# Kernel optimization log

Hardware: AMD Instinct MI355X
Metric: run time of the kernel (lower is better)

The kernel has to match this reference:

```python
import jax, jax.numpy as jnp
import numpy as np

B, N, D = 8, 2048, 256
TOP_K_INST = 512
TOP_K_REL = 32
EPS = 1e-5  # F.layer_norm default eps


def setup_inputs() -> dict:
    key = jax.random.key(0)
    kq, kk = jax.random.split(key)
    q = jax.random.normal(kq, (B, N, D), dtype=jnp.float32)
    k = jax.random.normal(kk, (B, N, D), dtype=jnp.float32)
    return {"q": q, "k": k}


def _forward(q, k):
    # raw attention scores [B,N,N] (returned un-normalized, like scores1 in torch)
    scores1 = jnp.einsum('bid,bjd->bij', q, k)
    probs = jax.nn.softmax(scores1, axis=-1)
    # top-k instances by softmax self-score on the diagonal, sorted ascending
    diag = jnp.diagonal(probs, axis1=-2, axis2=-1)                      # [B,N]
    inst_idx = jnp.sort(jax.lax.top_k(diag, TOP_K_INST)[1], axis=-1)    # [B,K]
    # gather selected rows then selected columns -> [B,K,K]
    sel = jnp.take_along_axis(probs, inst_idx[:, :, None], axis=1)      # [B,K,N]
    rel = jnp.take_along_axis(sel, inst_idx[:, None, :], axis=2)        # [B,K,K]
    # mask diagonal with large value (torch uses 1e9) before relationship topk
    rel = jnp.where(jnp.eye(TOP_K_INST, dtype=bool)[None, :, :], 1e9, rel)
    # top-R relationship columns per row; torch.where recovers them in
    # ascending column order, so sort to match
    rel_idx = jnp.sort(jax.lax.top_k(rel, TOP_K_REL)[1], axis=-1)       # [B,K,R]
    b, K, R = rel_idx.shape
    rows = jnp.broadcast_to(jnp.arange(K)[None, :, None], (b, K, R)).reshape(b, K * R)
    cols = rel_idx.reshape(b, K * R)
    subj = jnp.take_along_axis(inst_idx, rows, axis=-1)                 # [B,K*R]
    obj = jnp.take_along_axis(inst_idx, cols, axis=-1)                  # [B,K*R]
    batch_ids = jnp.broadcast_to(jnp.arange(b)[:, None], (b, K * R))
    soi = jnp.stack([batch_ids, subj, obj], axis=-1)                    # [B,K*R,3]
    # relationship embeds: q[subject] + q[object], then layernorm (no affine)
    subj_e = jnp.take_along_axis(q, subj[:, :, None], axis=1)           # [B,K*R,D]
    obj_e = jnp.take_along_axis(q, obj[:, :, None], axis=1)
    rel_e = subj_e + obj_e
    mu = jnp.mean(rel_e, axis=-1, keepdims=True)
    var = jnp.var(rel_e, axis=-1, keepdims=True)  # biased, matches F.layer_norm
    rel_e = (rel_e - mu) * jax.lax.rsqrt(var + EPS)
    return scores1, soi, rel_e


def reference(q, k):
    return _forward(q, k)
```

## Files before the change

kernel.cpp:

```cpp
#include <hip/hip_runtime.h>
#include <math.h>

#define BATCH 8
#define N 2048
#define D 256
#define K_INST 512
#define K_REL 32
#define PAIRS_PER_B (K_INST * K_REL)

__device__ __forceinline__ unsigned short f2h_u(float f) {
  _Float16 h = (_Float16)f;
  return __builtin_bit_cast(unsigned short, h);
}
__device__ __forceinline__ float h2f_u(unsigned short u) {
  return (float)__builtin_bit_cast(_Float16, u);
}

__global__ __launch_bounds__(256)
void split_f16(const float* __restrict__ q, const float* __restrict__ k,
               unsigned short* __restrict__ qhs, unsigned short* __restrict__ qh,
               unsigned short* __restrict__ ql, unsigned short* __restrict__ kh,
               unsigned short* __restrict__ kl) {
  const int E4 = BATCH * N * D / 4;
  for (int i = blockIdx.x * blockDim.x + threadIdx.x; i < 2 * E4;
       i += gridDim.x * blockDim.x) {
    const bool isK = i >= E4;
    const int j = isK ? (i - E4) : i;
    const float4 v = ((const float4*)(isK ? k : q))[j];
    ushort4 h, l;
    h.x = f2h_u(v.x); h.y = f2h_u(v.y); h.z = f2h_u(v.z); h.w = f2h_u(v.w);
    l.x = f2h_u(2048.0f * (v.x - h2f_u(h.x)));
    l.y = f2h_u(2048.0f * (v.y - h2f_u(h.y)));
    l.z = f2h_u(2048.0f * (v.z - h2f_u(h.z)));
    l.w = f2h_u(2048.0f * (v.w - h2f_u(h.w)));
    if (isK) {
      ((ushort4*)kh)[j] = h;
      ((ushort4*)kl)[j] = l;
    } else {
      ushort4 hs;
      hs.x = f2h_u(2048.0f * h2f_u(h.x));
      hs.y = f2h_u(2048.0f * h2f_u(h.y));
      hs.z = f2h_u(2048.0f * h2f_u(h.z));
      hs.w = f2h_u(2048.0f * h2f_u(h.w));
      ((ushort4*)qhs)[j] = hs;
      ((ushort4*)qh)[j] = h;
      ((ushort4*)ql)[j] = l;
    }
  }
}

#define TM 128
#define TN 128
#define TK 32

typedef _Float16 f16x8 __attribute__((ext_vector_type(8)));
typedef float f32x4 __attribute__((ext_vector_type(4)));

__device__ __forceinline__ void load_lds16(const void* g, void* l) {
  __builtin_amdgcn_global_load_lds(
      (const __attribute__((address_space(1))) void*)g,
      (__attribute__((address_space(3))) void*)l, 16, 0, 0);
}

__global__ __launch_bounds__(256, 3)
void gemm_qkT_mfma(const unsigned short* __restrict__ qhs,
                   const unsigned short* __restrict__ qh,
                   const unsigned short* __restrict__ ql,
                   const unsigned short* __restrict__ kh,
                   const unsigned short* __restrict__ kl,
                   float* __restrict__ out) {
  const int bz = blockIdx.z;
  const int row0 = blockIdx.y * TM;
  const int col0 = blockIdx.x * TN;
  const size_t tb = (size_t)bz * N * D;

  __shared__ unsigned short Ahs[TM * TK], Ah[TM * TK], Al[TM * TK],
                            Bh[TM * TK], Bl[TM * TK];

  const int tid = threadIdx.x;
  const int lane = tid & 63;
  const int w = tid >> 6;
  const int wr = w >> 1, wc = w & 1;
  const int fr = lane & 15;
  const int g = lane >> 4;
  const int slot8 = ((g ^ (lane & 3)) << 3);

  int r_st[2], k_st[2];
#pragma unroll
  for (int i = 0; i < 2; i++) {
    const int b = ((w * 2 + i) << 10) + lane * 16;
    const int r = b >> 6;
    const int s = (b >> 4) & 3;
    r_st[i] = r;
    k_st[i] = (s ^ (r & 3)) * 8;
  }

  f32x4 acc[4][4];
#pragma unroll
  for (int m = 0; m < 4; m++)
#pragma unroll
    for (int n = 0; n < 4; n++) acc[m][n] = (f32x4){0.f, 0.f, 0.f, 0.f};

  for (int kt = 0; kt < D; kt += TK) {
    __syncthreads();
#pragma unroll
    for (int i = 0; i < 2; i++) {
      const size_t aoff = tb + (size_t)(row0 + r_st[i]) * D + kt + k_st[i];
      const size_t boff = tb + (size_t)(col0 + r_st[i]) * D + kt + k_st[i];
      const int ldsoff = (w * 2 + i) * 512;
      load_lds16(qhs + aoff, &Ahs[ldsoff]);
      load_lds16(qh  + aoff, &Ah[ldsoff]);
      load_lds16(ql  + aoff, &Al[ldsoff]);
      load_lds16(kh  + boff, &Bh[ldsoff]);
      load_lds16(kl  + boff, &Bl[ldsoff]);
    }
    __syncthreads();

    f16x8 ahs[4], ah[4], al[4];
#pragma unroll
    for (int m = 0; m < 4; m++) {
      const int idx = (wr * 64 + m * 16 + fr) * TK + slot8;
      ahs[m] = *(const f16x8*)&Ahs[idx];
      ah[m] = *(const f16x8*)&Ah[idx];
      al[m] = *(const f16x8*)&Al[idx];
    }
#pragma unroll
    for (int n = 0; n < 4; n++) {
      const int idx = (wc * 64 + n * 16 + fr) * TK + slot8;
      const f16x8 bhf = *(const f16x8*)&Bh[idx];
      const f16x8 blf = *(const f16x8*)&Bl[idx];
#pragma unroll
      for (int m = 0; m < 4; m++) {
        acc[m][n] = __builtin_amdgcn_mfma_f32_16x16x32_f16(ahs[m], bhf, acc[m][n], 0, 0, 0);
        acc[m][n] = __builtin_amdgcn_mfma_f32_16x16x32_f16(ah[m], blf, acc[m][n], 0, 0, 0);
        acc[m][n] = __builtin_amdgcn_mfma_f32_16x16x32_f16(al[m], bhf, acc[m][n], 0, 0, 0);
      }
    }
  }

  float* O = out + (size_t)bz * N * N;
  const float inv2048 = 1.0f / 2048.0f;
#pragma unroll
  for (int m = 0; m < 4; m++) {
#pragma unroll
    for (int r4 = 0; r4 < 4; r4++) {
      float* orow =
          &O[(size_t)(row0 + wr * 64 + m * 16 + g * 4 + r4) * N + col0 + wc * 64 + fr];
#pragma unroll
      for (int n = 0; n < 4; n++) orow[n * 16] = acc[m][n][r4] * inv2048;
    }
  }
}

__global__ __launch_bounds__(256)
void row_stats(const float* __restrict__ scores, float* __restrict__ m_out,
               float* __restrict__ s_out, float* __restrict__ diag_out) {
  const int row = blockIdx.x;
  const float* srow = scores + (size_t)row * N;
  const float4* r4 = (const float4*)srow;
  const int t = threadIdx.x;
  const int lane = t & 63, wid = t >> 6;
  float4 v0 = r4[t];
  float4 v1 = r4[t + 256];
  float mx = fmaxf(fmaxf(fmaxf(v0.x, v0.y), fmaxf(v0.z, v0.w)),
                   fmaxf(fmaxf(v1.x, v1.y), fmaxf(v1.z, v1.w)));
  __shared__ float redm[4], reds[4], bc[1];
#pragma unroll
  for (int o = 32; o > 0; o >>= 1) mx = fmaxf(mx, __shfl_down(mx, o));
  if (lane == 0) redm[wid] = mx;
  __syncthreads();
  if (t == 0) bc[0] = fmaxf(fmaxf(redm[0], redm[1]), fmaxf(redm[2], redm[3]));
  __syncthreads();
  const float m = bc[0];
  float s = expf(v0.x - m) + expf(v0.y - m) + expf(v0.z - m) + expf(v0.w - m)
          + expf(v1.x - m) + expf(v1.y - m) + expf(v1.z - m) + expf(v1.w - m);
#pragma unroll
  for (int o = 32; o > 0; o >>= 1) s += __shfl_down(s, o);
  if (lane == 0) reds[wid] = s;
  __syncthreads();
  if (t == 0) {
    float S = reds[0] + reds[1] + reds[2] + reds[3];
    int i = row & (N - 1);
    float sii = srow[i];
    m_out[row] = m;
    s_out[row] = S;
    diag_out[row] = expf(sii - m) / S;
  }
}

__global__ __launch_bounds__(1024)
void topk_inst(const float* __restrict__ diag, int* __restrict__ inst) {
  const int b = blockIdx.x;
  __shared__ float v[2048];
  __shared__ int id[2048];
  __shared__ int sel[K_INST];
  const int tid = threadIdx.x;
  for (int e = tid; e < 2048; e += 1024) { v[e] = diag[b * N + e]; id[e] = e; }
  __syncthreads();
  for (int k = 2; k <= 2048; k <<= 1) {
    for (int j = k >> 1; j > 0; j >>= 1) {
      const int p = tid;
      int i = 2 * p - (p & (j - 1));
      int ixj = i | j;
      float va = v[i], vb = v[ixj];
      int ia = id[i], ib = id[ixj];
      bool a_first = (va > vb) || (va == vb && ia < ib);
      bool up = ((i & k) == 0);
      if (up != a_first) { v[i] = vb; v[ixj] = va; id[i] = ib; id[ixj] = ia; }
      __syncthreads();
    }
  }
  if (tid < K_INST) sel[tid] = id[tid];
  __syncthreads();
  for (int k = 2; k <= K_INST; k <<= 1) {
    for (int j = k >> 1; j > 0; j >>= 1) {
      if (tid < 256) {
        int p = tid;
        int i = 2 * p - (p & (j - 1));
        int ixj = i | j;
        int a = sel[i], c = sel[ixj];
        bool a_first = a < c;
        bool up = ((i & k) == 0);
        if (up != a_first) { sel[i] = c; sel[ixj] = a; }
      }
      __syncthreads();
    }
  }
  if (tid < K_INST) inst[b * K_INST + tid] = sel[tid];
}

__global__ __launch_bounds__(256)
void rel_topk(const float* __restrict__ scores, const int* __restrict__ inst,
              float* __restrict__ soi_out, int* __restrict__ pairs) {
  const int blk = blockIdx.x;
  const int b = blk >> 9;
  const int r = blk & 511;
  __shared__ unsigned long long kv[K_INST];
  __shared__ int selc[K_REL];
  __shared__ int sortedc[K_REL];
  const int tid = threadIdx.x;
  const int subj = inst[b * K_INST + r];
  const float* srow = scores + ((size_t)b * N + subj) * N;
  for (int e = tid; e < K_INST; e += 256) {
    unsigned int fb;
    if (e == r) {
      fb = 0xFFFFFFFFu;
    } else {
      const int col = inst[b * K_INST + e];
      unsigned int u = __float_as_uint(srow[col]);
      fb = (u >> 31) ? ~u : (u | 0x80000000u);
    }
    kv[e] = ((unsigned long long)fb << 32) | (unsigned int)(K_INST - 1 - e);
  }
  __syncthreads();
  for (int k = 2; k <= K_INST; k <<= 1) {
    for (int j = k >> 1; j > 0; j >>= 1) {
      int p = tid;
      int i = 2 * p - (p & (j - 1));
      int ixj = i | j;
      unsigned long long a = kv[i], c = kv[ixj];
      bool up = ((i & k) == 0);
      if (up == (a < c)) { kv[i] = c; kv[ixj] = a; }
      __syncthreads();
    }
  }
  if (tid < K_REL)
    selc[tid] = K_INST - 1 - (int)(kv[tid] & 0xFFFFFFFFu);
  __syncthreads();
  if (tid < K_REL) {
    int myc = selc[tid];
    int rank = 0;
#pragma unroll
    for (int p2 = 0; p2 < K_REL; p2++) rank += (selc[p2] < myc);
    sortedc[rank] = myc;
  }
  __syncthreads();
  if (tid < K_REL) {
    int cc = sortedc[tid];
    int obj = inst[b * K_INST + cc];
    size_t pidx = (size_t)b * PAIRS_PER_B + (size_t)r * K_REL + tid;
    soi_out[pidx * 3 + 0] = (float)b;
    soi_out[pidx * 3 + 1] = (float)subj;
    soi_out[pidx * 3 + 2] = (float)obj;
    pairs[pidx * 2 + 0] = subj;
    pairs[pidx * 2 + 1] = obj;
  }
}

__global__ __launch_bounds__(256)
void rel_embed(const float* __restrict__ q, const int* __restrict__ pairs,
               float* __restrict__ out) {
  const size_t p = (size_t)blockIdx.x * 4 + (threadIdx.x >> 6);
  const int lane = threadIdx.x & 63;
  const int b = (int)(p >> 14);
  const int subj = pairs[p * 2], obj = pairs[p * 2 + 1];
  const float* qs = q + ((size_t)b * N + subj) * D;
  const float* qo = q + ((size_t)b * N + obj) * D;
  const float4 a = *(const float4*)(qs + lane * 4);
  const float4 c = *(const float4*)(qo + lane * 4);
  float4 e = make_float4(a.x + c.x, a.y + c.y, a.z + c.z, a.w + c.w);
  float s = e.x + e.y + e.z + e.w;
#pragma unroll
  for (int o = 32; o > 0; o >>= 1) s += __shfl_down(s, o);
  const float mu = __shfl(s, 0) * (1.0f / D);
  float4 dv = make_float4(e.x - mu, e.y - mu, e.z - mu, e.w - mu);
  float s2 = dv.x * dv.x + dv.y * dv.y + dv.z * dv.z + dv.w * dv.w;
#pragma unroll
  for (int o = 32; o > 0; o >>= 1) s2 += __shfl_down(s2, o);
  const float var = __shfl(s2, 0) * (1.0f / D);
  const float r = rsqrtf(var + 1e-5f);
  *(float4*)(out + p * D + lane * 4) =
      make_float4(dv.x * r, dv.y * r, dv.z * r, dv.w * r);
}

extern "C" void kernel_launch(void* const* d_in, const int* in_sizes, int n_in,
                              void* d_out, int out_size, void* d_ws, size_t ws_size,
                              hipStream_t stream) {
  const float* q = (const float*)d_in[0];
  const float* k = (const float*)d_in[1];
  float* out = (float*)d_out;

  float* scores = out;
  float* soi = out + (size_t)BATCH * N * N;
  float* rele = soi + (size_t)BATCH * PAIRS_PER_B * 3;

  float* m_arr = (float*)d_ws;
  float* s_arr = m_arr + BATCH * N;
  float* diag = s_arr + BATCH * N;
  int* inst = (int*)(diag + BATCH * N);
  int* pairs = inst + BATCH * K_INST;

  unsigned short* qhs = (unsigned short*)rele;
  unsigned short* qh = qhs + (size_t)BATCH * N * D;
  unsigned short* ql = qh + (size_t)BATCH * N * D;
  unsigned short* kh = ql + (size_t)BATCH * N * D;
  unsigned short* kl = kh + (size_t)BATCH * N * D;

  split_f16<<<4096, 256, 0, stream>>>(q, k, qhs, qh, ql, kh, kl);
  gemm_qkT_mfma<<<dim3(N / TN, N / TM, BATCH), 256, 0, stream>>>(qhs, qh, ql, kh, kl, scores);
  row_stats<<<BATCH * N, 256, 0, stream>>>(scores, m_arr, s_arr, diag);
  topk_inst<<<BATCH, 1024, 0, stream>>>(diag, inst);
  rel_topk<<<BATCH * K_INST, 256, 0, stream>>>(scores, inst, soi, pairs);
  rel_embed<<<BATCH * PAIRS_PER_B / 4, 256, 0, stream>>>(q, pairs, rele);
}
```

Before: 420.9 us.

## Fuse softmax row max/sum partials into GEMM epilogue and drop prescaled q copy

The GEMM epilogue now computes per-tile row max and exp-sum and writes them as partials. A small combine kernel merges those partials and computes the softmax diagonal, which replaces the row_stats pass that reread the whole score matrix. The prescaled high-half q buffer is removed and rebuilt in registers by an f16 multiply, which cuts split-kernel writes and GEMM loads. In exchange the epilogue does extra shuffle and exp work, uses fast __expf, and adds a block-wide sync.

```diff
diff --git a/kernel.cpp b/kernel.cpp
--- a/kernel.cpp
+++ b/kernel.cpp
@@ -18,9 +18,8 @@
 
 __global__ __launch_bounds__(256)
 void split_f16(const float* __restrict__ q, const float* __restrict__ k,
-               unsigned short* __restrict__ qhs, unsigned short* __restrict__ qh,
-               unsigned short* __restrict__ ql, unsigned short* __restrict__ kh,
-               unsigned short* __restrict__ kl) {
+               unsigned short* __restrict__ qh, unsigned short* __restrict__ ql,
+               unsigned short* __restrict__ kh, unsigned short* __restrict__ kl) {
   const int E4 = BATCH * N * D / 4;
   for (int i = blockIdx.x * blockDim.x + threadIdx.x; i < 2 * E4;
        i += gridDim.x * blockDim.x) {
@@ -33,19 +32,8 @@
     l.y = f2h_u(2048.0f * (v.y - h2f_u(h.y)));
     l.z = f2h_u(2048.0f * (v.z - h2f_u(h.z)));
     l.w = f2h_u(2048.0f * (v.w - h2f_u(h.w)));
-    if (isK) {
-      ((ushort4*)kh)[j] = h;
-      ((ushort4*)kl)[j] = l;
-    } else {
-      ushort4 hs;
-      hs.x = f2h_u(2048.0f * h2f_u(h.x));
-      hs.y = f2h_u(2048.0f * h2f_u(h.y));
-      hs.z = f2h_u(2048.0f * h2f_u(h.z));
-      hs.w = f2h_u(2048.0f * h2f_u(h.w));
-      ((ushort4*)qhs)[j] = hs;
-      ((ushort4*)qh)[j] = h;
-      ((ushort4*)ql)[j] = l;
-    }
+    ((ushort4*)(isK ? kh : qh))[j] = h;
+    ((ushort4*)(isK ? kl : ql))[j] = l;
   }
 }
 
@@ -63,19 +51,19 @@
 }
 
 __global__ __launch_bounds__(256, 3)
-void gemm_qkT_mfma(const unsigned short* __restrict__ qhs,
-                   const unsigned short* __restrict__ qh,
+void gemm_qkT_mfma(const unsigned short* __restrict__ qh,
                    const unsigned short* __restrict__ ql,
                    const unsigned short* __restrict__ kh,
                    const unsigned short* __restrict__ kl,
-                   float* __restrict__ out) {
+                   float* __restrict__ out,
+                   float* __restrict__ pm, float* __restrict__ ps) {
   const int bz = blockIdx.z;
   const int row0 = blockIdx.y * TM;
   const int col0 = blockIdx.x * TN;
   const size_t tb = (size_t)bz * N * D;
 
-  __shared__ unsigned short Ahs[TM * TK], Ah[TM * TK], Al[TM * TK],
-                            Bh[TM * TK], Bl[TM * TK];
+  __shared__ unsigned short Ah[TM * TK], Al[TM * TK], Bh[TM * TK], Bl[TM * TK];
+  __shared__ float redm[2][TM], reds[2][TM];
 
   const int tid = threadIdx.x;
   const int lane = tid & 63;
@@ -108,11 +96,10 @@
       const size_t aoff = tb + (size_t)(row0 + r_st[i]) * D + kt + k_st[i];
       const size_t boff = tb + (size_t)(col0 + r_st[i]) * D + kt + k_st[i];
       const int ldsoff = (w * 2 + i) * 512;
-      load_lds16(qhs + aoff, &Ahs[ldsoff]);
-      load_lds16(qh  + aoff, &Ah[ldsoff]);
-      load_lds16(ql  + aoff, &Al[ldsoff]);
-      load_lds16(kh  + boff, &Bh[ldsoff]);
-      load_lds16(kl  + boff, &Bl[ldsoff]);
+      load_lds16(qh + aoff, &Ah[ldsoff]);
+      load_lds16(ql + aoff, &Al[ldsoff]);
+      load_lds16(kh + boff, &Bh[ldsoff]);
+      load_lds16(kl + boff, &Bl[ldsoff]);
     }
     __syncthreads();
 
@@ -120,9 +107,9 @@
 #pragma unroll
     for (int m = 0; m < 4; m++) {
       const int idx = (wr * 64 + m * 16 + fr) * TK + slot8;
-      ahs[m] = *(const f16x8*)&Ahs[idx];
       ah[m] = *(const f16x8*)&Ah[idx];
       al[m] = *(const f16x8*)&Al[idx];
+      ahs[m] = ah[m] * (_Float16)2048.0f;
     }
 #pragma unroll
     for (int n = 0; n < 4; n++) {
@@ -144,48 +131,54 @@
   for (int m = 0; m < 4; m++) {
 #pragma unroll
     for (int r4 = 0; r4 < 4; r4++) {
+      float v0 = acc[m][0][r4] * inv2048;
+      float v1 = acc[m][1][r4] * inv2048;
+      float v2 = acc[m][2][r4] * inv2048;
+      float v3 = acc[m][3][r4] * inv2048;
       float* orow =
           &O[(size_t)(row0 + wr * 64 + m * 16 + g * 4 + r4) * N + col0 + wc * 64 + fr];
-#pragma unroll
-      for (int n = 0; n < 4; n++) orow[n * 16] = acc[m][n][r4] * inv2048;
-    }
+      orow[0] = v0; orow[16] = v1; orow[32] = v2; orow[48] = v3;
+      float mx = fmaxf(fmaxf(v0, v1), fmaxf(v2, v3));
+#pragma unroll
+      for (int o = 1; o < 16; o <<= 1) mx = fmaxf(mx, __shfl_xor(mx, o));
+      float se = __expf(v0 - mx) + __expf(v1 - mx) + __expf(v2 - mx) + __expf(v3 - mx);
+#pragma unroll
+      for (int o = 1; o < 16; o <<= 1) se += __shfl_xor(se, o);
+      if (fr == 0) {
+        const int rrow = wr * 64 + m * 16 + g * 4 + r4;
+        redm[wc][rrow] = mx;
+        reds[wc][rrow] = se;
+      }
+    }
+  }
+  __syncthreads();
+  if (tid < TM) {
+    const float m0 = redm[0][tid], m1 = redm[1][tid];
+    const float M = fmaxf(m0, m1);
+    const float S = reds[0][tid] * __expf(m0 - M) + reds[1][tid] * __expf(m1 - M);
+    const size_t idx = ((size_t)bz * N + row0 + tid) * 16 + blockIdx.x;
+    pm[idx] = M;
+    ps[idx] = S;
   }
 }
 
 __global__ __launch_bounds__(256)
-void row_stats(const float* __restrict__ scores, float* __restrict__ m_out,
-               float* __restrict__ s_out, float* __restrict__ diag_out) {
-  const int row = blockIdx.x;
-  const float* srow = scores + (size_t)row * N;
-  const float4* r4 = (const float4*)srow;
-  const int t = threadIdx.x;
-  const int lane = t & 63, wid = t >> 6;
-  float4 v0 = r4[t];
-  float4 v1 = r4[t + 256];
-  float mx = fmaxf(fmaxf(fmaxf(v0.x, v0.y), fmaxf(v0.z, v0.w)),
-                   fmaxf(fmaxf(v1.x, v1.y), fmaxf(v1.z, v1.w)));
-  __shared__ float redm[4], reds[4], bc[1];
-#pragma unroll
-  for (int o = 32; o > 0; o >>= 1) mx = fmaxf(mx, __shfl_down(mx, o));
-  if (lane == 0) redm[wid] = mx;
-  __syncthreads();
-  if (t == 0) bc[0] = fmaxf(fmaxf(redm[0], redm[1]), fmaxf(redm[2], redm[3]));
-  __syncthreads();
-  const float m = bc[0];
-  float s = expf(v0.x - m) + expf(v0.y - m) + expf(v0.z - m) + expf(v0.w - m)
-          + expf(v1.x - m) + expf(v1.y - m) + expf(v1.z - m) + expf(v1.w - m);
-#pragma unroll
-  for (int o = 32; o > 0; o >>= 1) s += __shfl_down(s, o);
-  if (lane == 0) reds[wid] = s;
-  __syncthreads();
-  if (t == 0) {
-    float S = reds[0] + reds[1] + reds[2] + reds[3];
-    int i = row & (N - 1);
-    float sii = srow[i];
-    m_out[row] = m;
-    s_out[row] = S;
-    diag_out[row] = expf(sii - m) / S;
-  }
+void row_combine(const float* __restrict__ pm, const float* __restrict__ ps,
+                 const float* __restrict__ scores, float* __restrict__ diag) {
+  const int row = blockIdx.x * 256 + threadIdx.x;
+  float pmv[16];
+  float M = -INFINITY;
+#pragma unroll
+  for (int j = 0; j < 16; j++) {
+    pmv[j] = pm[(size_t)row * 16 + j];
+    M = fmaxf(M, pmv[j]);
+  }
+  float S = 0.f;
+#pragma unroll
+  for (int j = 0; j < 16; j++) S += ps[(size_t)row * 16 + j] * __expf(pmv[j] - M);
+  const int i = row & (N - 1);
+  const float sii = scores[(size_t)row * N + i];
+  diag[row] = __expf(sii - M) / S;
 }
 
 __global__ __launch_bounds__(1024)
@@ -324,21 +317,20 @@
   float* soi = out + (size_t)BATCH * N * N;
   float* rele = soi + (size_t)BATCH * PAIRS_PER_B * 3;
 
-  float* m_arr = (float*)d_ws;
-  float* s_arr = m_arr + BATCH * N;
-  float* diag = s_arr + BATCH * N;
+  float* diag = (float*)d_ws;
   int* inst = (int*)(diag + BATCH * N);
   int* pairs = inst + BATCH * K_INST;
 
-  unsigned short* qhs = (unsigned short*)rele;
-  unsigned short* qh = qhs + (size_t)BATCH * N * D;
+  unsigned short* qh = (unsigned short*)rele;
   unsigned short* ql = qh + (size_t)BATCH * N * D;
   unsigned short* kh = ql + (size_t)BATCH * N * D;
   unsigned short* kl = kh + (size_t)BATCH * N * D;
-
-  split_f16<<<4096, 256, 0, stream>>>(q, k, qhs, qh, ql, kh, kl);
-  gemm_qkT_mfma<<<dim3(N / TN, N / TM, BATCH), 256, 0, stream>>>(qhs, qh, ql, kh, kl, scores);
-  row_stats<<<BATCH * N, 256, 0, stream>>>(scores, m_arr, s_arr, diag);
+  float* pm = (float*)(kl + (size_t)BATCH * N * D);
+  float* ps = pm + (size_t)BATCH * N * 16;
+
+  split_f16<<<4096, 256, 0, stream>>>(q, k, qh, ql, kh, kl);
+  gemm_qkT_mfma<<<dim3(N / TN, N / TM, BATCH), 256, 0, stream>>>(qh, ql, kh, kl, scores, pm, ps);
+  row_combine<<<BATCH * N / 256, 256, 0, stream>>>(pm, ps, scores, diag);
   topk_inst<<<BATCH, 1024, 0, stream>>>(diag, inst);
   rel_topk<<<BATCH * K_INST, 256, 0, stream>>>(scores, inst, soi, pairs);
   rel_embed<<<BATCH * PAIRS_PER_B / 4, 256, 0, stream>>>(q, pairs, rele);
```

Result: no change. 420.5 us (-0.1%).
